# Performance work log

Measured on AMD Instinct MI355X. Metric: run time of the kernel, lower is better.

## Reference

```python
import jax, jax.numpy as jnp
import numpy as np

B, T, C, D = 16, 4096, 1024, 64  # batch, tokens, d_model, head dim (d_model // n_heads)


def setup_inputs() -> dict:
    key = jax.random.key(0)
    kx, kq, kk, kv = jax.random.split(key, 4)
    scale_w = 1.0 / np.sqrt(C)
    return {
        "x": jax.random.normal(kx, (B, T, C), dtype=jnp.float32),
        "Wq": jax.random.normal(kq, (C, D), dtype=jnp.float32) * scale_w,
        "Wk": jax.random.normal(kk, (C, D), dtype=jnp.float32) * scale_w,
        "Wv": jax.random.normal(kv, (C, D), dtype=jnp.float32) * scale_w,
    }


def reference(x, Wq, Wk, Wv):
    # q, k, v: [B, T, D]; bias-free linear projections
    q = jnp.einsum("btc,cd->btd", x, Wq)
    k = jnp.einsum("btc,cd->btd", x, Wk)
    v = jnp.einsum("btc,cd->btd", x, Wv)
    # scores scaled by C**-0.5 (full d_model, matching the original module)
    scale = jnp.asarray(C, x.dtype) ** -0.5
    wei = jnp.einsum("bqd,bkd->bqk", q, k) * scale  # [B, T, T]
    wei = jax.nn.softmax(wei, axis=-1)
    # dropout is identity in eval mode
    return jnp.einsum("bqk,bkd->bqd", wei, v)  # [B, T, D]
```

## Files before the change

### kernel.cpp

```cpp
#include <hip/hip_runtime.h>
#include <stdint.h>

#define B_ 16
#define T_ 4096
#define C_ 1024
#define D_ 64
#define LOG2E 1.4426950408889634f

using f32x4 = __attribute__((ext_vector_type(4))) float;
using bf16x8 = __attribute__((ext_vector_type(8))) short;

__device__ __forceinline__ unsigned short f2bf(float x) {
  union { float f; uint32_t u; } v; v.f = x;
  uint32_t r = (v.u + 0x7fffu + ((v.u >> 16) & 1u)) >> 16;
  return (unsigned short)r;
}

__device__ __forceinline__ uint32_t cvtpk(float lo, float hi) {
  uint32_t r;
  asm("v_cvt_pk_bf16_f32 %0, %1, %2" : "=v"(r) : "v"(lo), "v"(hi));
  return r;
}

__device__ __forceinline__ void gload16(const void* gptr, void* lptr) {
  auto g = (const __attribute__((address_space(1))) uint32_t*)(uintptr_t)gptr;
  auto l = (__attribute__((address_space(3))) uint32_t*)(uintptr_t)lptr;
  __builtin_amdgcn_global_load_lds(g, l, 16, 0, 0);
}

#define SYNC_VM4()  asm volatile("s_waitcnt vmcnt(4)\ns_barrier" ::: "memory")
#define SYNC_VM0()  asm volatile("s_waitcnt vmcnt(0)\ns_barrier" ::: "memory")
#define SYNC_LGKM() asm volatile("s_waitcnt lgkmcnt(0)\ns_barrier" ::: "memory")

__global__ void k_prep(const float* __restrict__ Wq, const float* __restrict__ Wk,
                       const float* __restrict__ Wv, unsigned short* __restrict__ Wt) {
  int idx = blockIdx.x * 256 + threadIdx.x;
  int n = idx >> 10, k = idx & 1023;
  const float* W = (n < 64) ? Wq : (n < 128 ? Wk : Wv);
  Wt[idx] = f2bf(W[(size_t)k * 64 + (n & 63)]);
}

__global__ __launch_bounds__(256) void k_proj(const float* __restrict__ X,
                                              const unsigned short* __restrict__ Wt,
                                              unsigned short* __restrict__ Qo,
                                              unsigned short* __restrict__ Ko,
                                              unsigned short* __restrict__ Vto) {
  __shared__ float Xs[128 * 32];
  __shared__ unsigned short Ws[192 * 32];
  const int tid = threadIdx.x;
  const int wave = tid >> 6, lane = tid & 63;
  const int g = lane >> 4, c = lane & 15;
  const int m0 = blockIdx.x * 128;

  f32x4 acc[2][12];
#pragma unroll
  for (int a = 0; a < 2; ++a)
#pragma unroll
    for (int b2 = 0; b2 < 12; ++b2) acc[a][b2] = f32x4{0.f, 0.f, 0.f, 0.f};

  const int xrow = tid >> 3, xseg = tid & 7;
  const int wrow = tid >> 2, wseg = tid & 3;

  for (int step = 0; step < 32; ++step) {
    const int k0 = step * 32;
#pragma unroll
    for (int p = 0; p < 4; ++p) {
      int row = p * 32 + xrow;
      int seg = xseg ^ (row & 7);
      gload16(X + (size_t)(m0 + row) * C_ + k0 + seg * 4,
              (char*)Xs + p * 4096 + wave * 1024);
    }
#pragma unroll
    for (int p = 0; p < 3; ++p) {
      int n = p * 64 + wrow;
      int seg = wseg ^ ((n >> 1) & 3);
      gload16(Wt + (size_t)n * C_ + k0 + seg * 8,
              (char*)Ws + p * 4096 + wave * 1024);
    }
    __syncthreads();

    bf16x8 af[2];
#pragma unroll
    for (int mi = 0; mi < 2; ++mi) {
      int row = wave * 32 + mi * 16 + c;
      int sub = g * 2;
      f32x4 x0 = *(const f32x4*)((const char*)Xs + row * 128 + (((sub) ^ (row & 7)) * 16));
      f32x4 x1 = *(const f32x4*)((const char*)Xs + row * 128 + (((sub + 1) ^ (row & 7)) * 16));
      bf16x8 t;
      t[0] = (short)f2bf(x0[0]); t[1] = (short)f2bf(x0[1]);
      t[2] = (short)f2bf(x0[2]); t[3] = (short)f2bf(x0[3]);
      t[4] = (short)f2bf(x1[0]); t[5] = (short)f2bf(x1[1]);
      t[6] = (short)f2bf(x1[2]); t[7] = (short)f2bf(x1[3]);
      af[mi] = t;
    }
#pragma unroll
    for (int ni = 0; ni < 12; ++ni) {
      int n = ni * 16 + c;
      bf16x8 bf = *(const bf16x8*)((const char*)Ws + n * 64 + ((g ^ ((n >> 1) & 3)) * 16));
      acc[0][ni] = __builtin_amdgcn_mfma_f32_16x16x32_bf16(af[0], bf, acc[0][ni], 0, 0, 0);
      acc[1][ni] = __builtin_amdgcn_mfma_f32_16x16x32_bf16(af[1], bf, acc[1][ni], 0, 0, 0);
    }
    __syncthreads();
  }

  const int b = m0 >> 12;
#pragma unroll
  for (int mi = 0; mi < 2; ++mi) {
    int r0 = m0 + wave * 32 + mi * 16 + g * 4;
#pragma unroll
    for (int ni = 0; ni < 12; ++ni) {
      int col = ni * 16 + c;
      if (ni < 4) {
#pragma unroll
        for (int i = 0; i < 4; ++i)
          Qo[(size_t)(r0 + i) * D_ + col] = f2bf(acc[mi][ni][i] * (0.03125f * LOG2E));
      } else if (ni < 8) {
        int d = col - 64;
#pragma unroll
        for (int i = 0; i < 4; ++i)
          Ko[(size_t)(r0 + i) * D_ + d] = f2bf(acc[mi][ni][i]);
      } else {
        int d = col - 128;
        int tt = r0 & (T_ - 1);
        ushort4 pk;
        pk.x = f2bf(acc[mi][ni][0]); pk.y = f2bf(acc[mi][ni][1]);
        pk.z = f2bf(acc[mi][ni][2]); pk.w = f2bf(acc[mi][ni][3]);
        *(ushort4*)(Vto + (size_t)b * (D_ * T_) + (size_t)d * T_ + tt) = pk;
      }
    }
  }
}

__global__ __launch_bounds__(256, 2) void k_attn(const unsigned short* __restrict__ Qi,
                                                 const unsigned short* __restrict__ Ki,
                                                 const unsigned short* __restrict__ Vti,
                                                 float* __restrict__ Out) {
  __shared__ unsigned short Ks[2][64 * 64];
  __shared__ unsigned short Vs[2][64 * 64];
  __shared__ unsigned short Ps[4][2][16 * 64];

  const int tid = threadIdx.x;
  const int wave = tid >> 6, lane = tid & 63;
  const int g = lane >> 4, c = lane & 15;
  const int b = blockIdx.y;
  const int q0 = blockIdx.x * 128;
  const int qb = q0 + wave * 32;

  const unsigned short* Qb = Qi + (size_t)b * T_ * D_;
  const unsigned short* Kb = Ki + (size_t)b * T_ * D_;
  const unsigned short* Vb = Vti + (size_t)b * D_ * T_;

  bf16x8 qf[2][2];
#pragma unroll
  for (int qq = 0; qq < 2; ++qq)
#pragma unroll
    for (int kk = 0; kk < 2; ++kk)
      qf[qq][kk] = *(const bf16x8*)(Qb + (size_t)(qb + qq * 16 + c) * D_ + kk * 32 + g * 8);

  bf16x8 ones;
#pragma unroll
  for (int i = 0; i < 8; ++i) ones[i] = (short)0x3F80;

  f32x4 o[2][4], l4[2];
#pragma unroll
  for (int qq = 0; qq < 2; ++qq) {
    l4[qq] = f32x4{0.f, 0.f, 0.f, 0.f};
#pragma unroll
    for (int nd = 0; nd < 4; ++nd) o[qq][nd] = f32x4{0.f, 0.f, 0.f, 0.f};
  }

  const int srow = tid >> 3, sseg = tid & 7;

#define STAGE(BUF, KT)                                                          \
  do {                                                                          \
    _Pragma("unroll") for (int p = 0; p < 2; ++p) {                             \
      int row = p * 32 + srow;                                                  \
      int seg = sseg ^ (row & 7);                                               \
      gload16(Kb + (size_t)((KT) * 64 + row) * D_ + seg * 8,                    \
              (char*)&Ks[BUF][0] + p * 4096 + wave * 1024);                     \
      gload16(Vb + (size_t)row * T_ + (KT) * 64 + seg * 8,                      \
              (char*)&Vs[BUF][0] + p * 4096 + wave * 1024);                     \
    }                                                                           \
  } while (0)

#define TILE_COMPUTE(CUR)                                                       \
  do {                                                                          \
    f32x4 s[2][4];                                                              \
    _Pragma("unroll") for (int qq = 0; qq < 2; ++qq)                            \
        _Pragma("unroll") for (int tt = 0; tt < 4; ++tt)                        \
            s[qq][tt] = f32x4{0.f, 0.f, 0.f, 0.f};                              \
    __builtin_amdgcn_s_setprio(1);                                              \
    _Pragma("unroll") for (int kk = 0; kk < 2; ++kk) {                          \
      _Pragma("unroll") for (int tt = 0; tt < 4; ++tt) {                        \
        int trow = tt * 16 + c;                                                 \
        bf16x8 kf = *(const bf16x8*)((const char*)&Ks[CUR][0] + trow * 128 +    \
                                     (((kk * 4 + g) ^ (trow & 7)) * 16));       \
        s[0][tt] = __builtin_amdgcn_mfma_f32_16x16x32_bf16(kf, qf[0][kk], s[0][tt], 0, 0, 0); \
        s[1][tt] = __builtin_amdgcn_mfma_f32_16x16x32_bf16(kf, qf[1][kk], s[1][tt], 0, 0, 0); \
      }                                                                         \
    }                                                                           \
    __builtin_amdgcn_s_setprio(0);                                              \
        \
    _Pragma("unroll") for (int qq = 0; qq < 2; ++qq) {                          \
      char* pwq = (char*)&Ps[wave][qq][0];                                      \
      _Pragma("unroll") for (int tt = 0; tt < 4; ++tt) {                        \
        float p0 = exp2f(s[qq][tt][0]);                                         \
        float p1 = exp2f(s[qq][tt][1]);                                         \
        float p2 = exp2f(s[qq][tt][2]);                                         \
        float p3 = exp2f(s[qq][tt][3]);                                         \
        uint32_t w0 = cvtpk(p0, p1);                                            \
        uint32_t w1 = cvtpk(p2, p3);                                            \
        unsigned long long v = (unsigned long long)w0 | ((unsigned long long)w1 << 32); \
        *(unsigned long long*)(pwq + c * 128 + (((2 * tt + (g >> 1)) ^ (c & 7)) * 16) + \
                               (g & 1) * 8) = v;                                \
      }                                                                         \
    }                                                                           \
           \
    asm volatile("s_waitcnt lgkmcnt(0)" ::: "memory");                          \
    __builtin_amdgcn_sched_barrier(0);                                          \
    bf16x8 pb[2][2];                                                            \
    _Pragma("unroll") for (int qq = 0; qq < 2; ++qq)                            \
        _Pragma("unroll") for (int kk = 0; kk < 2; ++kk)                        \
            pb[qq][kk] = *(const bf16x8*)((char*)&Ps[wave][qq][0] + c * 128 +   \
                                          (((4 * kk + g) ^ (c & 7)) * 16));     \
    __builtin_amdgcn_s_setprio(1);                                              \
    _Pragma("unroll") for (int kk = 0; kk < 2; ++kk) {                          \
      _Pragma("unroll") for (int nd = 0; nd < 4; ++nd) {                        \
        int drow = nd * 16 + c;                                                 \
        bf16x8 vf = *(const bf16x8*)((const char*)&Vs[CUR][0] + drow * 128 +    \
                                     (((kk * 4 + g) ^ (drow & 7)) * 16));       \
        o[0][nd] = __builtin_amdgcn_mfma_f32_16x16x32_bf16(vf, pb[0][kk], o[0][nd], 0, 0, 0); \
        o[1][nd] = __builtin_amdgcn_mfma_f32_16x16x32_bf16(vf, pb[1][kk], o[1][nd], 0, 0, 0); \
      }                                                                         \
      l4[0] = __builtin_amdgcn_mfma_f32_16x16x32_bf16(ones, pb[0][kk], l4[0], 0, 0, 0); \
      l4[1] = __builtin_amdgcn_mfma_f32_16x16x32_bf16(ones, pb[1][kk], l4[1], 0, 0, 0); \
    }                                                                           \
    __builtin_amdgcn_s_setprio(0);                                              \
  } while (0)

  STAGE(0, 0);
  int cur = 0;
  for (int kt = 0; kt < 63; ++kt) {
    STAGE(cur ^ 1, kt + 1);
    SYNC_VM4();
    TILE_COMPUTE(cur);
    SYNC_LGKM();
    cur ^= 1;
  }
  SYNC_VM0();
  TILE_COMPUTE(cur);

#pragma unroll
  for (int qq = 0; qq < 2; ++qq) {
    float inv = 1.0f / l4[qq][0];
    float* Ob = Out + ((size_t)b * T_ + qb + qq * 16 + c) * D_;
#pragma unroll
    for (int nd = 0; nd < 4; ++nd) {
      f32x4 t = o[qq][nd];
      t[0] *= inv; t[1] *= inv; t[2] *= inv; t[3] *= inv;
      *(f32x4*)(Ob + nd * 16 + 4 * g) = t;
    }
  }
#undef STAGE
#undef TILE_COMPUTE
}

extern "C" void kernel_launch(void* const* d_in, const int* in_sizes, int n_in,
                              void* d_out, int out_size, void* d_ws, size_t ws_size,
                              hipStream_t stream) {
  const float* x  = (const float*)d_in[0];
  const float* Wq = (const float*)d_in[1];
  const float* Wk = (const float*)d_in[2];
  const float* Wv = (const float*)d_in[3];
  float* out = (float*)d_out;
  char* ws = (char*)d_ws;
  unsigned short* Wt = (unsigned short*)(ws);
  unsigned short* Qb = (unsigned short*)(ws + (1u << 20));
  unsigned short* Kb = (unsigned short*)(ws + (9u << 20));
  unsigned short* Vt = (unsigned short*)(ws + (17u << 20));

  k_prep<<<768, 256, 0, stream>>>(Wq, Wk, Wv, Wt);
  k_proj<<<512, 256, 0, stream>>>(x, Wt, Qb, Kb, Vt);
  k_attn<<<dim3(T_ / 128, B_), 256, 0, stream>>>(Qb, Kb, Vt, out);
}
```

Before: 187.6 us.

## Switch attention to 32x32x16 MFMA and keep P in registers via permlane swap

Rewrites the attention inner loop to use 32x32x16 bf16 MFMA tiles instead of 16x16x32, so each wave computes its 32 queries with fewer, larger matrix instructions. The softmax probabilities are repacked into the B-operand layout with v_permlane32_swap instead of a round trip through per-wave LDS scratch, which removes the P shared-memory buffer, its writes, reads and the lgkmcnt wait. The trade-off is higher register pressure from 16-wide accumulators and tighter dependence on exact lane-layout correctness of the permlane repacking.

```diff
diff --git a/kernel.cpp b/kernel.cpp
--- a/kernel.cpp
+++ b/kernel.cpp
@@ -8,7 +8,9 @@
 #define LOG2E 1.4426950408889634f
 
 using f32x4 = __attribute__((ext_vector_type(4))) float;
+using f32x16 = __attribute__((ext_vector_type(16))) float;
 using bf16x8 = __attribute__((ext_vector_type(8))) short;
+union U8 { uint32_t u[4]; bf16x8 v; };
 
 __device__ __forceinline__ unsigned short f2bf(float x) {
   union { float f; uint32_t u; } v; v.f = x;
@@ -20,6 +22,10 @@
   uint32_t r;
   asm("v_cvt_pk_bf16_f32 %0, %1, %2" : "=v"(r) : "v"(lo), "v"(hi));
   return r;
+}
+
+__device__ __forceinline__ void plswap(uint32_t& a, uint32_t& b) {
+  asm volatile("v_permlane32_swap_b32 %0, %1" : "+v"(a), "+v"(b));
 }
 
 __device__ __forceinline__ void gload16(const void* gptr, void* lptr) {
@@ -137,37 +143,30 @@
                                                  float* __restrict__ Out) {
   __shared__ unsigned short Ks[2][64 * 64];
   __shared__ unsigned short Vs[2][64 * 64];
-  __shared__ unsigned short Ps[4][2][16 * 64];
 
   const int tid = threadIdx.x;
   const int wave = tid >> 6, lane = tid & 63;
-  const int g = lane >> 4, c = lane & 15;
+  const int ql = lane & 31;
+  const int hi = lane >> 5;
   const int b = blockIdx.y;
-  const int q0 = blockIdx.x * 128;
-  const int qb = q0 + wave * 32;
+  const int qb = blockIdx.x * 128 + wave * 32;
 
   const unsigned short* Qb = Qi + (size_t)b * T_ * D_;
   const unsigned short* Kb = Ki + (size_t)b * T_ * D_;
   const unsigned short* Vb = Vti + (size_t)b * D_ * T_;
 
-  bf16x8 qf[2][2];
-#pragma unroll
-  for (int qq = 0; qq < 2; ++qq)
-#pragma unroll
-    for (int kk = 0; kk < 2; ++kk)
-      qf[qq][kk] = *(const bf16x8*)(Qb + (size_t)(qb + qq * 16 + c) * D_ + kk * 32 + g * 8);
+  bf16x8 qf[4];
+#pragma unroll
+  for (int ks = 0; ks < 4; ++ks)
+    qf[ks] = *(const bf16x8*)(Qb + (size_t)(qb + ql) * D_ + ks * 16 + 8 * hi);
 
   bf16x8 ones;
 #pragma unroll
   for (int i = 0; i < 8; ++i) ones[i] = (short)0x3F80;
 
-  f32x4 o[2][4], l4[2];
-#pragma unroll
-  for (int qq = 0; qq < 2; ++qq) {
-    l4[qq] = f32x4{0.f, 0.f, 0.f, 0.f};
-#pragma unroll
-    for (int nd = 0; nd < 4; ++nd) o[qq][nd] = f32x4{0.f, 0.f, 0.f, 0.f};
-  }
+  f32x16 o0, o1, l4;
+#pragma unroll
+  for (int i = 0; i < 16; ++i) { o0[i] = 0.f; o1[i] = 0.f; l4[i] = 0.f; }
 
   const int srow = tid >> 3, sseg = tid & 7;
 
@@ -183,57 +182,46 @@
     }                                                                           \
   } while (0)
 
+#define PACK_TB(SC, PB_EVEN, PB_ODD)                                            \
+  do {                                                                          \
+    float p_[16];                                                               \
+    _Pragma("unroll") for (int r = 0; r < 16; ++r) p_[r] = exp2f((SC)[r]);      \
+    uint32_t w00 = cvtpk(p_[0], p_[1]),   w01 = cvtpk(p_[2], p_[3]);            \
+    uint32_t w10 = cvtpk(p_[4], p_[5]),   w11 = cvtpk(p_[6], p_[7]);            \
+    uint32_t w20 = cvtpk(p_[8], p_[9]),   w21 = cvtpk(p_[10], p_[11]);          \
+    uint32_t w30 = cvtpk(p_[12], p_[13]), w31 = cvtpk(p_[14], p_[15]);          \
+    plswap(w00, w10); plswap(w01, w11);                                         \
+    plswap(w20, w30); plswap(w21, w31);                                         \
+    { U8 t_; t_.u[0] = w00; t_.u[1] = w01; t_.u[2] = w10; t_.u[3] = w11;        \
+      PB_EVEN = t_.v; }                                                         \
+    { U8 t_; t_.u[0] = w20; t_.u[1] = w21; t_.u[2] = w30; t_.u[3] = w31;        \
+      PB_ODD = t_.v; }                                                          \
+  } while (0)
+
 #define TILE_COMPUTE(CUR)                                                       \
   do {                                                                          \
-    f32x4 s[2][4];                                                              \
-    _Pragma("unroll") for (int qq = 0; qq < 2; ++qq)                            \
-        _Pragma("unroll") for (int tt = 0; tt < 4; ++tt)                        \
-            s[qq][tt] = f32x4{0.f, 0.f, 0.f, 0.f};                              \
+    f32x16 s0, s1;                                                              \
+    _Pragma("unroll") for (int i = 0; i < 16; ++i) { s0[i] = 0.f; s1[i] = 0.f; }\
     __builtin_amdgcn_s_setprio(1);                                              \
-    _Pragma("unroll") for (int kk = 0; kk < 2; ++kk) {                          \
-      _Pragma("unroll") for (int tt = 0; tt < 4; ++tt) {                        \
-        int trow = tt * 16 + c;                                                 \
-        bf16x8 kf = *(const bf16x8*)((const char*)&Ks[CUR][0] + trow * 128 +    \
-                                     (((kk * 4 + g) ^ (trow & 7)) * 16));       \
-        s[0][tt] = __builtin_amdgcn_mfma_f32_16x16x32_bf16(kf, qf[0][kk], s[0][tt], 0, 0, 0); \
-        s[1][tt] = __builtin_amdgcn_mfma_f32_16x16x32_bf16(kf, qf[1][kk], s[1][tt], 0, 0, 0); \
-      }                                                                         \
+    _Pragma("unroll") for (int ks = 0; ks < 4; ++ks) {                          \
+      int sg = ((2 * ks + hi) ^ (ql & 7)) * 16;                                 \
+      bf16x8 kf0 = *(const bf16x8*)((const char*)&Ks[CUR][0] + ql * 128 + sg);  \
+      bf16x8 kf1 = *(const bf16x8*)((const char*)&Ks[CUR][0] + (32 + ql) * 128 + sg); \
+      s0 = __builtin_amdgcn_mfma_f32_32x32x16_bf16(kf0, qf[ks], s0, 0, 0, 0);   \
+      s1 = __builtin_amdgcn_mfma_f32_32x32x16_bf16(kf1, qf[ks], s1, 0, 0, 0);   \
     }                                                                           \
     __builtin_amdgcn_s_setprio(0);                                              \
-        \
-    _Pragma("unroll") for (int qq = 0; qq < 2; ++qq) {                          \
-      char* pwq = (char*)&Ps[wave][qq][0];                                      \
-      _Pragma("unroll") for (int tt = 0; tt < 4; ++tt) {                        \
-        float p0 = exp2f(s[qq][tt][0]);                                         \
-        float p1 = exp2f(s[qq][tt][1]);                                         \
-        float p2 = exp2f(s[qq][tt][2]);                                         \
-        float p3 = exp2f(s[qq][tt][3]);                                         \
-        uint32_t w0 = cvtpk(p0, p1);                                            \
-        uint32_t w1 = cvtpk(p2, p3);                                            \
-        unsigned long long v = (unsigned long long)w0 | ((unsigned long long)w1 << 32); \
-        *(unsigned long long*)(pwq + c * 128 + (((2 * tt + (g >> 1)) ^ (c & 7)) * 16) + \
-                               (g & 1) * 8) = v;                                \
-      }                                                                         \
-    }                                                                           \
-           \
-    asm volatile("s_waitcnt lgkmcnt(0)" ::: "memory");                          \
-    __builtin_amdgcn_sched_barrier(0);                                          \
-    bf16x8 pb[2][2];                                                            \
-    _Pragma("unroll") for (int qq = 0; qq < 2; ++qq)                            \
-        _Pragma("unroll") for (int kk = 0; kk < 2; ++kk)                        \
-            pb[qq][kk] = *(const bf16x8*)((char*)&Ps[wave][qq][0] + c * 128 +   \
-                                          (((4 * kk + g) ^ (c & 7)) * 16));     \
+    bf16x8 pb[4];                                                               \
+    PACK_TB(s0, pb[0], pb[1]);                                                  \
+    PACK_TB(s1, pb[2], pb[3]);                                                  \
     __builtin_amdgcn_s_setprio(1);                                              \
-    _Pragma("unroll") for (int kk = 0; kk < 2; ++kk) {                          \
-      _Pragma("unroll") for (int nd = 0; nd < 4; ++nd) {                        \
-        int drow = nd * 16 + c;                                                 \
-        bf16x8 vf = *(const bf16x8*)((const char*)&Vs[CUR][0] + drow * 128 +    \
-                                     (((kk * 4 + g) ^ (drow & 7)) * 16));       \
-        o[0][nd] = __builtin_amdgcn_mfma_f32_16x16x32_bf16(vf, pb[0][kk], o[0][nd], 0, 0, 0); \
-        o[1][nd] = __builtin_amdgcn_mfma_f32_16x16x32_bf16(vf, pb[1][kk], o[1][nd], 0, 0, 0); \
-      }                                                                         \
-      l4[0] = __builtin_amdgcn_mfma_f32_16x16x32_bf16(ones, pb[0][kk], l4[0], 0, 0, 0); \
-      l4[1] = __builtin_amdgcn_mfma_f32_16x16x32_bf16(ones, pb[1][kk], l4[1], 0, 0, 0); \
+    _Pragma("unroll") for (int s = 0; s < 4; ++s) {                             \
+      int sg = ((2 * s + hi) ^ (ql & 7)) * 16;                                  \
+      bf16x8 vf0 = *(const bf16x8*)((const char*)&Vs[CUR][0] + ql * 128 + sg);  \
+      bf16x8 vf1 = *(const bf16x8*)((const char*)&Vs[CUR][0] + (32 + ql) * 128 + sg); \
+      o0 = __builtin_amdgcn_mfma_f32_32x32x16_bf16(vf0, pb[s], o0, 0, 0, 0);    \
+      o1 = __builtin_amdgcn_mfma_f32_32x32x16_bf16(vf1, pb[s], o1, 0, 0, 0);    \
+      l4 = __builtin_amdgcn_mfma_f32_32x32x16_bf16(ones, pb[s], l4, 0, 0, 0);   \
     }                                                                           \
     __builtin_amdgcn_s_setprio(0);                                              \
   } while (0)
@@ -250,18 +238,18 @@
   SYNC_VM0();
   TILE_COMPUTE(cur);
 
-#pragma unroll
-  for (int qq = 0; qq < 2; ++qq) {
-    float inv = 1.0f / l4[qq][0];
-    float* Ob = Out + ((size_t)b * T_ + qb + qq * 16 + c) * D_;
-#pragma unroll
-    for (int nd = 0; nd < 4; ++nd) {
-      f32x4 t = o[qq][nd];
-      t[0] *= inv; t[1] *= inv; t[2] *= inv; t[3] *= inv;
-      *(f32x4*)(Ob + nd * 16 + 4 * g) = t;
-    }
+  float inv = 1.0f / l4[0];
+  float* Ob = Out + ((size_t)b * T_ + qb + ql) * D_;
+#pragma unroll
+  for (int rq = 0; rq < 4; ++rq) {
+    f32x4 t0, t1;
+#pragma unroll
+    for (int i = 0; i < 4; ++i) { t0[i] = o0[4 * rq + i] * inv; t1[i] = o1[4 * rq + i] * inv; }
+    *(f32x4*)(Ob + rq * 8 + hi * 4) = t0;
+    *(f32x4*)(Ob + 32 + rq * 8 + hi * 4) = t1;
   }
 #undef STAGE
+#undef PACK_TB
 #undef TILE_COMPUTE
 }
 
```

After: 186.3 us. About the same (-0.7%).
